# Kernel optimization log

Measured on AMD Instinct MI355X. Metric: run time of the kernel, lower is better.

## Reference

```python
import jax, jax.numpy as jnp
import numpy as np

N_ATOMS = 100000
N_EDGES = 1600000
N_GRAPHS = 64
N_BASIS = 128
N_FILTERS = 128
N_RBF = 32
N_INTER = 6
CUTOFF = 10.0
LOG2 = float(np.log(2.0))


def ssp(x):
    # shifted softplus
    return jax.nn.softplus(x) - LOG2


def setup_inputs() -> dict:
    key = jax.random.key(0)
    ks = jax.random.split(key, 24)
    s = 0.05
    inp = {
        "z": jax.random.randint(ks[0], (N_ATOMS,), 0, 100),
        "z_res": jax.random.randint(ks[1], (N_ATOMS,), 0, 100),
        "pos": jax.random.normal(ks[2], (N_ATOMS, 3), jnp.float32) * 5.0,
        "idx_i": jax.random.randint(ks[3], (N_EDGES,), 0, N_ATOMS),
        "idx_j": jax.random.randint(ks[4], (N_EDGES,), 0, N_ATOMS),
        "edge_attr": jax.random.randint(ks[5], (N_EDGES,), 0, 4),
        "batch": jnp.sort(jax.random.randint(ks[6], (N_ATOMS,), 0, N_GRAPHS)),
        "ele_emb": jax.random.normal(ks[7], (100, N_BASIS), jnp.float32) * s,
        "res_emb": jax.random.normal(ks[8], (100, N_BASIS), jnp.float32) * s,
        "edge_emb": jax.random.normal(ks[9], (4, N_RBF), jnp.float32) * s,
        "in2f_W": jax.random.normal(ks[10], (N_INTER, N_BASIS, N_FILTERS), jnp.float32) * s,
        "filt_W1": jax.random.normal(ks[11], (N_INTER, N_RBF, N_FILTERS), jnp.float32) * s,
        "filt_b1": jnp.zeros((N_INTER, N_FILTERS), jnp.float32),
        "filt_W2": jax.random.normal(ks[12], (N_INTER, N_FILTERS, N_FILTERS), jnp.float32) * s,
        "filt_b2": jnp.zeros((N_INTER, N_FILTERS), jnp.float32),
        "f2out_W1": jax.random.normal(ks[13], (N_INTER, N_FILTERS, N_BASIS), jnp.float32) * s,
        "f2out_b1": jnp.zeros((N_INTER, N_BASIS), jnp.float32),
        "f2out_W2": jax.random.normal(ks[14], (N_INTER, N_BASIS, N_BASIS), jnp.float32) * s,
        "f2out_b2": jnp.zeros((N_INTER, N_BASIS), jnp.float32),
        "head_W1": jax.random.normal(ks[15], (N_BASIS, N_BASIS), jnp.float32) * s,
        "head_b1": jnp.zeros((N_BASIS,), jnp.float32),
        "head_W2": jax.random.normal(ks[16], (N_BASIS, 1), jnp.float32) * s,
    }
    return inp


def _forward(z, z_res, pos, idx_i, idx_j, edge_attr, batch,
             ele_emb, res_emb, edge_emb,
             in2f_W, filt_W1, filt_b1, filt_W2, filt_b2,
             f2out_W1, f2out_b1, f2out_W2, f2out_b2,
             head_W1, head_b1, head_W2):
    # distances per edge
    r_ij = pos[idx_i] - pos[idx_j]                       # [E,3]
    d_ij = jnp.linalg.norm(r_ij, axis=1)                 # [E]

    # Gaussian RBF expansion: offsets linspace(0, cutoff, n_rbf)
    offsets = jnp.linspace(0.0, CUTOFF, N_RBF)
    width = offsets[1] - offsets[0]
    coeff = -0.5 / (width * width)
    f_ij = jnp.exp(coeff * (d_ij[:, None] - offsets[None, :]) ** 2)  # [E,R]
    f_ij = f_ij + edge_emb[edge_attr]

    # cosine cutoff
    rcut_ij = 0.5 * (jnp.cos(d_ij * jnp.pi / CUTOFF) + 1.0) * (d_ij < CUTOFF)

    # atom embeddings
    x = ele_emb[z] + res_emb[z_res]                      # [N,B]

    for i in range(N_INTER):
        xf = x @ in2f_W[i]                               # [N,F]
        Wij = ssp(f_ij @ filt_W1[i] + filt_b1[i]) @ filt_W2[i] + filt_b2[i]
        Wij = Wij * rcut_ij[:, None]                     # [E,F]
        x_ij = xf[idx_j] * Wij                           # gather + multiply
        agg = jax.ops.segment_sum(x_ij, idx_i, num_segments=N_ATOMS)  # scatter_add
        v = ssp(agg @ f2out_W1[i] + f2out_b1[i]) @ f2out_W2[i] + f2out_b2[i]
        x = x + v

    # L2 normalize then head
    h = x / jnp.maximum(jnp.linalg.norm(x, axis=-1, keepdims=True), 1e-12)
    h = jax.nn.silu(h) @ head_W1 + head_b1
    h = jax.nn.silu(h) @ head_W2                         # [N,1]
    new_y = jax.ops.segment_sum(h, batch, num_segments=N_GRAPHS)  # [G,1]
    return new_y.squeeze(-1)


def reference(z, z_res, pos, idx_i, idx_j, edge_attr, batch,
              ele_emb, res_emb, edge_emb,
              in2f_W, filt_W1, filt_b1, filt_W2, filt_b2,
              f2out_W1, f2out_b1, f2out_W2, f2out_b2,
              head_W1, head_b1, head_W2):
    return _forward(z, z_res, pos, idx_i, idx_j, edge_attr, batch,
                    ele_emb, res_emb, edge_emb,
                    in2f_W, filt_W1, filt_b1, filt_W2, filt_b2,
                    f2out_W1, f2out_b1, f2out_W2, f2out_b2,
                    head_W1, head_b1, head_W2)
```

## Files before the change

kernel.cpp:

```cpp
#include <hip/hip_runtime.h>
#include <hip/hip_bf16.h>
#include <math.h>

#define NB 128
#define NR 32
#define EPAD 40
#define HPAD 136
#define SCB 256


static constexpr float CUTOFF_F    = 10.0f;
static constexpr float RBF_STEP    = 10.0f / 31.0f;
static constexpr float RBF_COEFF   = -4.805f;
static constexpr float LOG2_F      = 0.69314718055994531f;
static constexpr float PI_OVER_CUT = 0.314159265358979f;

typedef __attribute__((ext_vector_type(8))) short bf16x8;
typedef __attribute__((ext_vector_type(2))) short bf16x2;
typedef __attribute__((ext_vector_type(4))) float f32x4;

__device__ __forceinline__ short f2bs(float x) {
    __hip_bfloat16 h = __float2bfloat16(x);
    return *reinterpret_cast<short*>(&h);
}
__device__ __forceinline__ float bs2f(unsigned short u) {
    unsigned int v = ((unsigned int)u) << 16;
    return __uint_as_float(v);
}
__device__ __forceinline__ float ssp_f(float v) {
    return fmaxf(v, 0.0f) + __logf(1.0f + __expf(-fabsf(v))) - LOG2_F;
}
__device__ __forceinline__ float silu_f(float v) {
    return v / (1.0f + __expf(-v));
}

__device__ __forceinline__ void atomic_pk_add_bf16(short* addr, float lo, float hi) {
#if __has_builtin(__builtin_amdgcn_global_atomic_fadd_v2bf16)
    typedef bf16x2 __attribute__((address_space(1))) *gptr;
    bf16x2 v;
    v[0] = f2bs(lo);
    v[1] = f2bs(hi);
    __builtin_amdgcn_global_atomic_fadd_v2bf16((gptr)(unsigned long long)addr, v);
#else
    unsigned int* w = (unsigned int*)addr;
    unsigned int old = *w, assumed;
    do {
        assumed = old;
        float fl = bs2f((unsigned short)(assumed & 0xffff)) + lo;
        float fh = bs2f((unsigned short)(assumed >> 16)) + hi;
        unsigned int nv = ((unsigned int)(unsigned short)f2bs(fh) << 16) |
                          (unsigned short)f2bs(fl);
        old = atomicCAS(w, assumed, nv);
    } while (old != assumed);
#endif
}

__device__ __forceinline__ void flush_pk(short* aggrow, const float* accum, int col) {
    bool even = ((col & 1) == 0);
#pragma unroll
    for (int q = 0; q < 4; q++) {
        float a = accum[2 * q], b = accum[2 * q + 1];
        float pa = __shfl_xor(a, 1);
        float pb = __shfl_xor(b, 1);
        int nbase = even ? (2 * q) * 16 + col : (2 * q + 1) * 16 + (col - 1);
        float lo = even ? a : pb;
        float hi = even ? pa : b;
        atomic_pk_add_bf16(aggrow + nbase, lo, hi);
    }
}

__global__ void transpose_cvt(const float* __restrict__ src, short* __restrict__ dst,
                              int R, int C, int total) {
    int t = blockIdx.x * blockDim.x + threadIdx.x;
    if (t >= total) return;
    int rc = R * C;
    int b = t / rc;
    int rem = t - b * rc;
    int c = rem / R;
    int r = rem - c * R;
    dst[t] = f2bs(src[(size_t)b * rc + (size_t)r * C + c]);
}

__global__ void edge_prep4(const float* __restrict__ pos,
                           const int* __restrict__ idx_i,
                           const int* __restrict__ idx_j,
                           float* __restrict__ d_ij,
                           int* __restrict__ hist,
                           int E) {
    int b0 = blockIdx.x * 1024 + threadIdx.x;
    int ia[4], ib[4];
    bool val[4];
#pragma unroll
    for (int k = 0; k < 4; k++) {
        int e = b0 + k * 256;
        val[k] = (e < E);
        ia[k] = val[k] ? idx_i[e] : 0;
        ib[k] = val[k] ? idx_j[e] : 0;
    }
    float ax[4], ay[4], az[4], bx[4], by[4], bz[4];
#pragma unroll
    for (int k = 0; k < 4; k++) {
        const float* pa = pos + ia[k] * 3;
        ax[k] = pa[0]; ay[k] = pa[1]; az[k] = pa[2];
    }
#pragma unroll
    for (int k = 0; k < 4; k++) {
        const float* pb = pos + ib[k] * 3;
        bx[k] = pb[0]; by[k] = pb[1]; bz[k] = pb[2];
    }
#pragma unroll
    for (int k = 0; k < 4; k++) {
        if (!val[k]) continue;
        float dx = ax[k] - bx[k], dy = ay[k] - by[k], dz = az[k] - bz[k];
        float d = sqrtf(dx * dx + dy * dy + dz * dz);
        d_ij[b0 + k * 256] = d;
        if (d < CUTOFF_F) atomicAdd(&hist[ia[k]], 1);
    }
}

__global__ __launch_bounds__(256) void scan_reduce(const int* __restrict__ hist,
                                                   int* __restrict__ partial, int N) {
    __shared__ int red[256];
    int b = blockIdx.x;
    int chunk = (N + SCB - 1) / SCB;
    int lo = b * chunk;
    int hi = min(lo + chunk, N);
    int s = 0;
    for (int i = lo + threadIdx.x; i < hi; i += 256) s += hist[i];
    red[threadIdx.x] = s;
    __syncthreads();
    for (int d = 128; d > 0; d >>= 1) {
        if (threadIdx.x < d) red[threadIdx.x] += red[threadIdx.x + d];
        __syncthreads();
    }
    if (threadIdx.x == 0) partial[b] = red[0];
}

__global__ __launch_bounds__(256) void scan_partials(int* __restrict__ partial) {
    __shared__ int sm[SCB];
    int t = threadIdx.x;
    sm[t] = partial[t];
    __syncthreads();
    for (int d = 1; d < SCB; d <<= 1) {
        int v = (t >= d) ? sm[t - d] : 0;
        __syncthreads();
        sm[t] += v;
        __syncthreads();
    }
    partial[t] = (t == 0) ? 0 : sm[t - 1];
}

__global__ __launch_bounds__(256) void scan_expand(const int* __restrict__ hist,
                                                   const int* __restrict__ partial,
                                                   int* __restrict__ cursor, int N) {
    __shared__ int tsum[256];
    int b = blockIdx.x;
    int chunk = (N + SCB - 1) / SCB;
    int lo = b * chunk;
    int hi = min(lo + chunk, N);
    int sub = (chunk + 255) / 256;
    int tlo = lo + threadIdx.x * sub;
    int thi = min(tlo + sub, hi);
    int s = 0;
    for (int i = tlo; i < thi; i++) s += hist[i];
    int t = threadIdx.x;
    tsum[t] = s;
    __syncthreads();
    for (int d = 1; d < 256; d <<= 1) {
        int v = (t >= d) ? tsum[t - d] : 0;
        __syncthreads();
        tsum[t] += v;
        __syncthreads();
    }
    int run = partial[b] + ((t == 0) ? 0 : tsum[t - 1]);
    for (int i = tlo; i < thi; i++) {
        cursor[i] = run;
        run += hist[i];
    }
}

__global__ void scatter_sorted4(const float* __restrict__ d_ij,
                                const int* __restrict__ idx_i,
                                const int* __restrict__ idx_j,
                                const int* __restrict__ edge_attr,
                                int* __restrict__ cursor,
                                float4* __restrict__ edata,
                                int* __restrict__ sIarr, int E) {
    int b0 = blockIdx.x * 1024 + threadIdx.x;
    float d[4]; int ii[4], jj[4], at[4]; bool act[4];
#pragma unroll
    for (int k = 0; k < 4; k++) {
        int e = b0 + k * 256;
        bool v = (e < E);
        d[k] = v ? d_ij[e] : 1e9f;
        act[k] = (d[k] < CUTOFF_F);
        ii[k] = act[k] ? idx_i[e] : 0;
        jj[k] = act[k] ? idx_j[e] : 0;
        at[k] = act[k] ? edge_attr[e] : 0;
    }
    int p[4];
#pragma unroll
    for (int k = 0; k < 4; k++)
        if (act[k]) p[k] = atomicAdd(&cursor[ii[k]], 1);
#pragma unroll
    for (int k = 0; k < 4; k++) {
        if (!act[k]) continue;
        float4 v;
        v.x = d[k];
        v.y = 0.5f * (__cosf(d[k] * PI_OVER_CUT) + 1.0f);
        v.z = __int_as_float(jj[k]);
        v.w = __int_as_float(at[k]);
        edata[p[k]] = v;
        sIarr[p[k]] = ii[k];
    }
}

__global__ void atom_embed(const int* __restrict__ z,
                           const int* __restrict__ z_res,
                           const float* __restrict__ ele_emb,
                           const float* __restrict__ res_emb,
                           float* __restrict__ x, int N) {
    int t = blockIdx.x * blockDim.x + threadIdx.x;
    if (t >= N * NB) return;
    int n = t >> 7, c = t & 127;
    x[t] = ele_emb[z[n] * NB + c] + res_emb[z_res[n] * NB + c];
}

__global__ __launch_bounds__(256, 4) void node_in2f_mfma(
    const float* __restrict__ x, const short* __restrict__ WT,
    short* __restrict__ xf, int N) {
    __shared__ __align__(16) short XA[64 * HPAD];
    int a0 = blockIdx.x * 64;
    int t = threadIdx.x;
#pragma unroll
    for (int c = 0; c < 4; c++) {
        int chunk = t + c * 256;
        int row = chunk >> 4;
        int col = (chunk & 15) * 8;
        short v[8];
        if (a0 + row < N) {
            const float* src = x + (size_t)(a0 + row) * NB + col;
            float4 f0 = *(const float4*)src;
            float4 f1 = *(const float4*)(src + 4);
            v[0] = f2bs(f0.x); v[1] = f2bs(f0.y); v[2] = f2bs(f0.z); v[3] = f2bs(f0.w);
            v[4] = f2bs(f1.x); v[5] = f2bs(f1.y); v[6] = f2bs(f1.z); v[7] = f2bs(f1.w);
        } else {
#pragma unroll
            for (int j = 0; j < 8; j++) v[j] = 0;
        }
        *(bf16x8*)&XA[row * HPAD + col] = *(bf16x8*)v;
    }
    __syncthreads();

    int wid = t >> 6, lane = t & 63;
    int quad = lane >> 4, col = lane & 15;
    int mrow = wid * 16 + col;

    f32x4 acc[8] = {};
#pragma unroll
    for (int kt = 0; kt < 4; kt++) {
        bf16x8 a = *(bf16x8*)&XA[mrow * HPAD + kt * 32 + quad * 8];
#pragma unroll
        for (int nt = 0; nt < 8; nt++) {
            bf16x8 b = *(const bf16x8*)&WT[(nt * 16 + col) * NB + kt * 32 + quad * 8];
            acc[nt] = __builtin_amdgcn_mfma_f32_16x16x32_bf16(a, b, acc[nt], 0, 0, 0);
        }
    }
#pragma unroll
    for (int nt = 0; nt < 8; nt++) {
        int cst = col * 8 + nt;
#pragma unroll
        for (int r = 0; r < 4; r++) {
            int m = wid * 16 + quad * 4 + r;
            if (a0 + m < N) xf[(size_t)(a0 + m) * NB + cst] = f2bs(acc[nt][r]);
        }
    }
}

__global__ __launch_bounds__(256, 4) void node_fused_mfma(
    short* __restrict__ agg,
    const short* __restrict__ W1T, const float* __restrict__ b1,
    const short* __restrict__ W2T, const float* __restrict__ b2,
    const short* __restrict__ WnT,
    float* __restrict__ x, short* __restrict__ xf, int N) {
    __shared__ __align__(16) short XA[64 * HPAD];
    __shared__ __align__(16) short H[64 * HPAD];
    int a0 = blockIdx.x * 64;
    int t = threadIdx.x;
#pragma unroll
    for (int c = 0; c < 4; c++) {
        int chunk = t + c * 256;
        int row = chunk >> 4;
        int col = (chunk & 15) * 8;
        bf16x8 v = {0, 0, 0, 0, 0, 0, 0, 0};
        if (a0 + row < N) {
            short* src = agg + (size_t)(a0 + row) * NB + col;
            v = *(const bf16x8*)src;
            *(bf16x8*)src = (bf16x8){0, 0, 0, 0, 0, 0, 0, 0};
        }
        *(bf16x8*)&XA[row * HPAD + col] = v;
    }
    __syncthreads();

    int wid = t >> 6, lane = t & 63;
    int quad = lane >> 4, col = lane & 15;
    int mrow = wid * 16 + col;

    {
        f32x4 acc[8] = {};
#pragma unroll
        for (int kt = 0; kt < 4; kt++) {
            bf16x8 a = *(bf16x8*)&XA[mrow * HPAD + kt * 32 + quad * 8];
#pragma unroll
            for (int nt = 0; nt < 8; nt++) {
                bf16x8 b = *(const bf16x8*)&W1T[(nt * 16 + col) * NB + kt * 32 + quad * 8];
                acc[nt] = __builtin_amdgcn_mfma_f32_16x16x32_bf16(a, b, acc[nt], 0, 0, 0);
            }
        }
#pragma unroll
        for (int nt = 0; nt < 8; nt++) {
            int n = nt * 16 + col;
            float bias = b1[n];
#pragma unroll
            for (int r = 0; r < 4; r++) {
                int m = wid * 16 + quad * 4 + r;
                H[m * HPAD + n] = f2bs(ssp_f(acc[nt][r] + bias));
            }
        }
    }
    __syncthreads();

    {
        f32x4 acc[8] = {};
#pragma unroll
        for (int kt = 0; kt < 4; kt++) {
            bf16x8 a = *(bf16x8*)&H[mrow * HPAD + kt * 32 + quad * 8];
#pragma unroll
            for (int nt = 0; nt < 8; nt++) {
                bf16x8 b = *(const bf16x8*)&W2T[(nt * 16 + col) * NB + kt * 32 + quad * 8];
                acc[nt] = __builtin_amdgcn_mfma_f32_16x16x32_bf16(a, b, acc[nt], 0, 0, 0);
            }
        }
#pragma unroll
        for (int nt = 0; nt < 8; nt++) {
            int n = nt * 16 + col;
            float bias = b2[n];
#pragma unroll
            for (int r = 0; r < 4; r++) {
                int m = wid * 16 + quad * 4 + r;
                float xn = 0.0f;
                if (a0 + m < N) {
                    size_t o = (size_t)(a0 + m) * NB + n;
                    xn = x[o] + acc[nt][r] + bias;
                    x[o] = xn;
                }
                XA[m * HPAD + n] = f2bs(xn);
            }
        }
    }
    __syncthreads();

    {
        f32x4 acc[8] = {};
#pragma unroll
        for (int kt = 0; kt < 4; kt++) {
            bf16x8 a = *(bf16x8*)&XA[mrow * HPAD + kt * 32 + quad * 8];
#pragma unroll
            for (int nt = 0; nt < 8; nt++) {
                bf16x8 b = *(const bf16x8*)&WnT[(nt * 16 + col) * NB + kt * 32 + quad * 8];
                acc[nt] = __builtin_amdgcn_mfma_f32_16x16x32_bf16(a, b, acc[nt], 0, 0, 0);
            }
        }
#pragma unroll
        for (int nt = 0; nt < 8; nt++) {
            int cst = col * 8 + nt;
#pragma unroll
            for (int r = 0; r < 4; r++) {
                int m = wid * 16 + quad * 4 + r;
                if (a0 + m < N) xf[(size_t)(a0 + m) * NB + cst] = f2bs(acc[nt][r]);
            }
        }
    }
}

__global__ __launch_bounds__(256, 4) void node_out_head_mfma(
    const short* __restrict__ agg,
    const short* __restrict__ W1T, const float* __restrict__ b1,
    const short* __restrict__ W2T, const float* __restrict__ b2,
    const float* __restrict__ x, const int* __restrict__ batch,
    const short* __restrict__ hW1T, const float* __restrict__ hb1,
    const float* __restrict__ hW2,
    float* __restrict__ out, int N) {
    __shared__ __align__(16) short XA[64 * HPAD];
    __shared__ __align__(16) short H[64 * HPAD];
    __shared__ int sbat[64];
    __shared__ float rowval[64];
    int a0 = blockIdx.x * 64;
    int t = threadIdx.x;

    if (t < 64) sbat[t] = (a0 + t < N) ? batch[a0 + t] : -1;
#pragma unroll
    for (int c = 0; c < 4; c++) {
        int chunk = t + c * 256;
        int row = chunk >> 4;
        int col = (chunk & 15) * 8;
        bf16x8 v = {0, 0, 0, 0, 0, 0, 0, 0};
        if (a0 + row < N) v = *(const bf16x8*)&agg[(size_t)(a0 + row) * NB + col];
        *(bf16x8*)&XA[row * HPAD + col] = v;
    }
    __syncthreads();

    int wid = t >> 6, lane = t & 63;
    int quad = lane >> 4, col = lane & 15;
    int mrow = wid * 16 + col;

    {
        f32x4 acc[8] = {};
#pragma unroll
        for (int kt = 0; kt < 4; kt++) {
            bf16x8 a = *(bf16x8*)&XA[mrow * HPAD + kt * 32 + quad * 8];
#pragma unroll
            for (int nt = 0; nt < 8; nt++) {
                bf16x8 b = *(const bf16x8*)&W1T[(nt * 16 + col) * NB + kt * 32 + quad * 8];
                acc[nt] = __builtin_amdgcn_mfma_f32_16x16x32_bf16(a, b, acc[nt], 0, 0, 0);
            }
        }
#pragma unroll
        for (int nt = 0; nt < 8; nt++) {
            int n = nt * 16 + col;
            float bias = b1[n];
#pragma unroll
            for (int r = 0; r < 4; r++) {
                int m = wid * 16 + quad * 4 + r;
                H[m * HPAD + n] = f2bs(ssp_f(acc[nt][r] + bias));
            }
        }
    }
    __syncthreads();

    float xnv[8][4];
    float ssq[4] = {0.f, 0.f, 0.f, 0.f};
    {
        f32x4 acc[8] = {};
#pragma unroll
        for (int kt = 0; kt < 4; kt++) {
            bf16x8 a = *(bf16x8*)&H[mrow * HPAD + kt * 32 + quad * 8];
#pragma unroll
            for (int nt = 0; nt < 8; nt++) {
                bf16x8 b = *(const bf16x8*)&W2T[(nt * 16 + col) * NB + kt * 32 + quad * 8];
                acc[nt] = __builtin_amdgcn_mfma_f32_16x16x32_bf16(a, b, acc[nt], 0, 0, 0);
            }
        }
#pragma unroll
        for (int nt = 0; nt < 8; nt++) {
            int n = nt * 16 + col;
            float bias = b2[n];
#pragma unroll
            for (int r = 0; r < 4; r++) {
                int m = wid * 16 + quad * 4 + r;
                float xn = 0.0f;
                if (a0 + m < N) xn = x[(size_t)(a0 + m) * NB + n] + acc[nt][r] + bias;
                xnv[nt][r] = xn;
                ssq[r] += xn * xn;
            }
        }
    }
#pragma unroll
    for (int r = 0; r < 4; r++) {
#pragma unroll
        for (int m = 1; m < 16; m <<= 1) ssq[r] += __shfl_xor(ssq[r], m);
    }
    float inv[4];
#pragma unroll
    for (int r = 0; r < 4; r++) inv[r] = 1.0f / fmaxf(sqrtf(ssq[r]), 1e-12f);
    __syncthreads();
#pragma unroll
    for (int nt = 0; nt < 8; nt++) {
        int n = nt * 16 + col;
#pragma unroll
        for (int r = 0; r < 4; r++) {
            int m = wid * 16 + quad * 4 + r;
            XA[m * HPAD + n] = f2bs(silu_f(xnv[nt][r] * inv[r]));
        }
    }
    __syncthreads();

    f32x4 acc[8] = {};
#pragma unroll
    for (int kt = 0; kt < 4; kt++) {
        bf16x8 a = *(bf16x8*)&XA[mrow * HPAD + kt * 32 + quad * 8];
#pragma unroll
        for (int nt = 0; nt < 8; nt++) {
            bf16x8 b = *(const bf16x8*)&hW1T[(nt * 16 + col) * NB + kt * 32 + quad * 8];
            acc[nt] = __builtin_amdgcn_mfma_f32_16x16x32_bf16(a, b, acc[nt], 0, 0, 0);
        }
    }
    float partial[4] = {0.f, 0.f, 0.f, 0.f};
#pragma unroll
    for (int nt = 0; nt < 8; nt++) {
        int n = nt * 16 + col;
        float bias = hb1[n];
        float w2 = hW2[n];
#pragma unroll
        for (int r = 0; r < 4; r++) partial[r] += silu_f(acc[nt][r] + bias) * w2;
    }
#pragma unroll
    for (int r = 0; r < 4; r++) {
#pragma unroll
        for (int d = 1; d < 16; d <<= 1) partial[r] += __shfl_xor(partial[r], d);
    }
    if (col == 0) {
#pragma unroll
        for (int r = 0; r < 4; r++) rowval[wid * 16 + quad * 4 + r] = partial[r];
    }
    __syncthreads();

    if (t < 64) {
        int b = sbat[t];
        bool headf = (b >= 0) && (t == 0 || sbat[t - 1] != b);
        if (headf) {
            float s = 0.0f;
            int rr = t;
            while (rr < 64 && sbat[rr] == b) { s += rowval[rr]; rr++; }
            atomicAdd(&out[b], s);
        }
    }
}

__global__ __launch_bounds__(256, 4) void edge_fused_mfma(
    const float4* __restrict__ edata, const int* __restrict__ sIarr,
    const int* __restrict__ rowend, int natoms,
    const float* __restrict__ edge_emb,
    const short* __restrict__ W1T, const float* __restrict__ b1,
    const short* __restrict__ W2T, const float* __restrict__ b2,
    const short* __restrict__ xf, short* __restrict__ agg) {
    __shared__ __align__(16) short fA[64 * EPAD];
    __shared__ __align__(16) short H[64 * HPAD];

    int t = threadIdx.x;
    int wid = t >> 6, lane = t & 63;
    int quad = lane >> 4, col = lane & 15;
    int base = blockIdx.x * 64;
    int wbase = base + wid * 16;
    int el16 = lane & 15;

    float4 ed = edata[wbase + el16];
    int sIv0 = sIarr[wbase + el16];
    int cnt = rowend[natoms - 1];
    if (base >= cnt) return;

    bool act = (wbase + el16) < cnt;
    float dv  = act ? ed.x : 1e9f;
    float rcv = act ? ed.y : 0.0f;
    int   jjv = act ? __float_as_int(ed.z) : 0;
    int   atv = act ? __float_as_int(ed.w) : 0;
    int   iiv = act ? sIv0 : 0;

    {
        int elA = lane >> 2;
        int r0 = (lane & 3) * 8;
        float d  = __shfl(dv, elA);
        int   at = __shfl(atv, elA);
        const float* em = edge_emb + at * NR + r0;
        short v[8];
#pragma unroll
        for (int j = 0; j < 8; j++) {
            float off = (float)(r0 + j) * RBF_STEP;
            float dd = d - off;
            v[j] = f2bs(__expf(RBF_COEFF * dd * dd) + em[j]);
        }
        *(bf16x8*)&fA[(wid * 16 + elA) * EPAD + r0] = *(bf16x8*)v;
    }

    int e0l = quad * 4;
    bf16x8 xv[4];
    const unsigned short* xg = (const unsigned short*)xf;
#pragma unroll
    for (int r = 0; r < 4; r++) {
        int jj = __shfl(jjv, e0l + r);
        xv[r] = *(const bf16x8*)&xg[(size_t)jj * NB + col * 8];
    }

    asm volatile("s_waitcnt lgkmcnt(0)" ::: "memory");
    __builtin_amdgcn_sched_barrier(0);

    int mrow = wid * 16 + col;

    {
        bf16x8 a1 = *(bf16x8*)&fA[mrow * EPAD + quad * 8];
        f32x4 acc[8];
#pragma unroll
        for (int nt = 0; nt < 8; nt++) {
            bf16x8 b = *(const bf16x8*)&W1T[(nt * 16 + col) * NR + quad * 8];
            acc[nt] = __builtin_amdgcn_mfma_f32_16x16x32_bf16(a1, b, (f32x4){0.f, 0.f, 0.f, 0.f}, 0, 0, 0);
        }
#pragma unroll
        for (int nt = 0; nt < 8; nt++) {
            int n = nt * 16 + col;
            float bias = b1[n];
#pragma unroll
            for (int r = 0; r < 4; r++) {
                int m = wid * 16 + quad * 4 + r;
                H[m * HPAD + n] = f2bs(ssp_f(acc[nt][r] + bias));
            }
        }
    }

    asm volatile("s_waitcnt lgkmcnt(0)" ::: "memory");
    __builtin_amdgcn_sched_barrier(0);

    f32x4 acc2[8] = {};
#pragma unroll
    for (int kt = 0; kt < 4; kt++) {
        bf16x8 a = *(bf16x8*)&H[mrow * HPAD + kt * 32 + quad * 8];
#pragma unroll
        for (int nt = 0; nt < 8; nt++) {
            bf16x8 b = *(const bf16x8*)&W2T[(nt * 16 + col) * NB + kt * 32 + quad * 8];
            acc2[nt] = __builtin_amdgcn_mfma_f32_16x16x32_bf16(a, b, acc2[nt], 0, 0, 0);
        }
    }

    float b2v[8];
#pragma unroll
    for (int nt = 0; nt < 8; nt++) b2v[nt] = b2[nt * 16 + col];

    int cur = __shfl(iiv, e0l);
    float accum[8] = {0.f, 0.f, 0.f, 0.f, 0.f, 0.f, 0.f, 0.f};
#pragma unroll
    for (int r = 0; r < 4; r++) {
        int ii = __shfl(iiv, e0l + r);
        float rc = __shfl(rcv, e0l + r);
        if (ii != cur) {
            flush_pk(agg + (size_t)cur * NB, accum, col);
#pragma unroll
            for (int nt = 0; nt < 8; nt++) accum[nt] = 0.f;
            cur = ii;
        }
#pragma unroll
        for (int nt = 0; nt < 8; nt++) {
            float w = (acc2[nt][r] + b2v[nt]) * rc;
            accum[nt] = fmaf(w, bs2f((unsigned short)xv[r][nt]), accum[nt]);
        }
    }
    flush_pk(agg + (size_t)cur * NB, accum, col);
}

extern "C" void kernel_launch(void* const* d_in, const int* in_sizes, int n_in,
                              void* d_out, int out_size, void* d_ws, size_t ws_size,
                              hipStream_t stream) {
    const int*   z        = (const int*)d_in[0];
    const int*   z_res    = (const int*)d_in[1];
    const float* pos      = (const float*)d_in[2];
    const int*   idx_i    = (const int*)d_in[3];
    const int*   idx_j    = (const int*)d_in[4];
    const int*   edge_attr= (const int*)d_in[5];
    const int*   batch    = (const int*)d_in[6];
    const float* ele_emb  = (const float*)d_in[7];
    const float* res_emb  = (const float*)d_in[8];
    const float* edge_emb = (const float*)d_in[9];
    const float* in2f_W   = (const float*)d_in[10];
    const float* filt_W1  = (const float*)d_in[11];
    const float* filt_b1  = (const float*)d_in[12];
    const float* filt_W2  = (const float*)d_in[13];
    const float* filt_b2  = (const float*)d_in[14];
    const float* f2out_W1 = (const float*)d_in[15];
    const float* f2out_b1 = (const float*)d_in[16];
    const float* f2out_W2 = (const float*)d_in[17];
    const float* f2out_b2 = (const float*)d_in[18];
    const float* head_W1  = (const float*)d_in[19];
    const float* head_b1  = (const float*)d_in[20];
    const float* head_W2  = (const float*)d_in[21];

    const int N = in_sizes[0];
    const int E = in_sizes[3];

    char* p = (char*)d_ws;
    size_t off = 0;
    auto carve = [&](size_t bytes) -> void* {
        void* q = p + off;
        off = (off + bytes + 255) & ~(size_t)255;
        return q;
    };
    float*  d_d      = (float*)carve((size_t)E * 4);
    float4* edata    = (float4*)carve((size_t)E * 16);
    int*    sIarr    = (int*)carve((size_t)E * 4);
    int*    hist     = (int*)carve((size_t)N * 4);
    int*    cursor   = (int*)carve((size_t)N * 4);
    int*    partial  = (int*)carve((size_t)SCB * 4);
    float*  x_buf    = (float*)carve((size_t)N * NB * 4);
    short*  xf_buf   = (short*)carve((size_t)N * NB * 2);
    short*  agg      = (short*)carve((size_t)N * NB * 2);
    short*  in2f_WT  = (short*)carve((size_t)6 * NB * NB * 2);
    short*  fW1T     = (short*)carve((size_t)6 * NR * NB * 2);
    short*  fW2T     = (short*)carve((size_t)6 * NB * NB * 2);
    short*  oW1T     = (short*)carve((size_t)6 * NB * NB * 2);
    short*  oW2T     = (short*)carve((size_t)6 * NB * NB * 2);
    short*  hW1T     = (short*)carve((size_t)NB * NB * 2);
    (void)ws_size;

    {
        int tot = 6 * NB * NB;
        transpose_cvt<<<(tot + 255) / 256, 256, 0, stream>>>(in2f_W, in2f_WT, NB, NB, tot);
        transpose_cvt<<<(tot + 255) / 256, 256, 0, stream>>>(filt_W2, fW2T, NB, NB, tot);
        transpose_cvt<<<(tot + 255) / 256, 256, 0, stream>>>(f2out_W1, oW1T, NB, NB, tot);
        transpose_cvt<<<(tot + 255) / 256, 256, 0, stream>>>(f2out_W2, oW2T, NB, NB, tot);
        int tot1 = 6 * NR * NB;
        transpose_cvt<<<(tot1 + 255) / 256, 256, 0, stream>>>(filt_W1, fW1T, NR, NB, tot1);
        int tot2 = NB * NB;
        transpose_cvt<<<(tot2 + 255) / 256, 256, 0, stream>>>(head_W1, hW1T, NB, NB, tot2);
    }

    hipMemsetAsync(hist, 0, (size_t)N * 4, stream);
    int nblk_e4 = (E + 1023) / 1024;
    edge_prep4<<<nblk_e4, 256, 0, stream>>>(pos, idx_i, idx_j, d_d, hist, E);
    scan_reduce<<<SCB, 256, 0, stream>>>(hist, partial, N);
    scan_partials<<<1, SCB, 0, stream>>>(partial);
    scan_expand<<<SCB, 256, 0, stream>>>(hist, partial, cursor, N);
    scatter_sorted4<<<nblk_e4, 256, 0, stream>>>(d_d, idx_i, idx_j, edge_attr,
                                                 cursor, edata, sIarr, E);

    atom_embed<<<(N * NB + 255) / 256, 256, 0, stream>>>(z, z_res, ele_emb, res_emb, x_buf, N);

    int nblk_atom64 = (N + 63) / 64;
    int nblk_edge = (E + 63) / 64;

    node_in2f_mfma<<<nblk_atom64, 256, 0, stream>>>(x_buf, in2f_WT, xf_buf, N);
    hipMemsetAsync(d_out, 0, (size_t)out_size * sizeof(float), stream);
    hipMemsetAsync(agg, 0, (size_t)N * NB * 2, stream);
    for (int i = 0; i < 6; i++) {
        edge_fused_mfma<<<nblk_edge, 256, 0, stream>>>(
            edata, sIarr, cursor, N, edge_emb,
            fW1T + (size_t)i * NR * NB, filt_b1 + (size_t)i * NB,
            fW2T + (size_t)i * NB * NB, filt_b2 + (size_t)i * NB,
            xf_buf, agg);
        if (i < 5) {
            node_fused_mfma<<<nblk_atom64, 256, 0, stream>>>(
                agg, oW1T + (size_t)i * NB * NB, f2out_b1 + (size_t)i * NB,
                oW2T + (size_t)i * NB * NB, f2out_b2 + (size_t)i * NB,
                in2f_WT + (size_t)(i + 1) * NB * NB,
                x_buf, xf_buf, N);
        } else {
            node_out_head_mfma<<<nblk_atom64, 256, 0, stream>>>(
                agg, oW1T + (size_t)i * NB * NB, f2out_b1 + (size_t)i * NB,
                oW2T + (size_t)i * NB * NB, f2out_b2 + (size_t)i * NB,
                x_buf, batch, hW1T, head_b1, head_W2,
                (float*)d_out, N);
        }
    }
}
```

Measured before the change: 2.208 ms.

## Process 32 edges per wave in edge kernel to reuse weight fragments

Each wave in the fused edge kernel now handles two 16-edge sub-tiles (128 edges per block), loading the W1/W2 B-fragments once and reusing them across both sub-tiles. The goal is to halve the global/cache weight loads per edge and amortize per-block setup. In exchange, register and LDS use roughly double, and launch bounds drop to 3 blocks per CU, which lowers occupancy for a kernel whose gathers are latency-bound.

```diff
diff --git a/kernel.cpp b/kernel.cpp
--- a/kernel.cpp
+++ b/kernel.cpp
@@ -527,29 +527,29 @@
     }
 }
 
-__global__ __launch_bounds__(256, 4) void edge_fused_mfma(
+__global__ __launch_bounds__(256, 3) void edge_fused_mfma(
     const float4* __restrict__ edata, const int* __restrict__ sIarr,
     const int* __restrict__ rowend, int natoms,
     const float* __restrict__ edge_emb,
     const short* __restrict__ W1T, const float* __restrict__ b1,
     const short* __restrict__ W2T, const float* __restrict__ b2,
     const short* __restrict__ xf, short* __restrict__ agg) {
-    __shared__ __align__(16) short fA[64 * EPAD];
-    __shared__ __align__(16) short H[64 * HPAD];
+    __shared__ __align__(16) short fA[128 * EPAD];
+    __shared__ __align__(16) short H[128 * HPAD];
 
     int t = threadIdx.x;
     int wid = t >> 6, lane = t & 63;
     int quad = lane >> 4, col = lane & 15;
-    int base = blockIdx.x * 64;
-    int wbase = base + wid * 16;
-    int el16 = lane & 15;
-
-    float4 ed = edata[wbase + el16];
-    int sIv0 = sIarr[wbase + el16];
+    int base = blockIdx.x * 128;
+    int wbase = base + wid * 32;
+    int el32 = lane & 31;
+
+    float4 ed = edata[wbase + el32];
+    int sIv0 = sIarr[wbase + el32];
     int cnt = rowend[natoms - 1];
     if (base >= cnt) return;
 
-    bool act = (wbase + el16) < cnt;
+    bool act = (wbase + el32) < cnt;
     float dv  = act ? ed.x : 1e9f;
     float rcv = act ? ed.y : 0.0f;
     int   jjv = act ? __float_as_int(ed.z) : 0;
@@ -557,51 +557,58 @@
     int   iiv = act ? sIv0 : 0;
 
     {
-        int elA = lane >> 2;
-        int r0 = (lane & 3) * 8;
+        int elA = lane >> 1;
+        int r0 = (lane & 1) * 16;
         float d  = __shfl(dv, elA);
         int   at = __shfl(atv, elA);
         const float* em = edge_emb + at * NR + r0;
-        short v[8];
-#pragma unroll
-        for (int j = 0; j < 8; j++) {
+        short v[16];
+#pragma unroll
+        for (int j = 0; j < 16; j++) {
             float off = (float)(r0 + j) * RBF_STEP;
             float dd = d - off;
             v[j] = f2bs(__expf(RBF_COEFF * dd * dd) + em[j]);
         }
-        *(bf16x8*)&fA[(wid * 16 + elA) * EPAD + r0] = *(bf16x8*)v;
-    }
-
-    int e0l = quad * 4;
-    bf16x8 xv[4];
+        short* dst = &fA[(wid * 32 + elA) * EPAD + r0];
+        *(bf16x8*)dst = *(bf16x8*)v;
+        *(bf16x8*)(dst + 8) = *(bf16x8*)(v + 8);
+    }
+
+    bf16x8 xv[2][4];
     const unsigned short* xg = (const unsigned short*)xf;
 #pragma unroll
-    for (int r = 0; r < 4; r++) {
-        int jj = __shfl(jjv, e0l + r);
-        xv[r] = *(const bf16x8*)&xg[(size_t)jj * NB + col * 8];
+    for (int s = 0; s < 2; s++) {
+#pragma unroll
+        for (int r = 0; r < 4; r++) {
+            int jj = __shfl(jjv, s * 16 + quad * 4 + r);
+            xv[s][r] = *(const bf16x8*)&xg[(size_t)jj * NB + col * 8];
+        }
     }
 
     asm volatile("s_waitcnt lgkmcnt(0)" ::: "memory");
     __builtin_amdgcn_sched_barrier(0);
 
-    int mrow = wid * 16 + col;
-
     {
-        bf16x8 a1 = *(bf16x8*)&fA[mrow * EPAD + quad * 8];
-        f32x4 acc[8];
-#pragma unroll
-        for (int nt = 0; nt < 8; nt++) {
-            bf16x8 b = *(const bf16x8*)&W1T[(nt * 16 + col) * NR + quad * 8];
-            acc[nt] = __builtin_amdgcn_mfma_f32_16x16x32_bf16(a1, b, (f32x4){0.f, 0.f, 0.f, 0.f}, 0, 0, 0);
-        }
-#pragma unroll
-        for (int nt = 0; nt < 8; nt++) {
-            int n = nt * 16 + col;
-            float bias = b1[n];
-#pragma unroll
-            for (int r = 0; r < 4; r++) {
-                int m = wid * 16 + quad * 4 + r;
-                H[m * HPAD + n] = f2bs(ssp_f(acc[nt][r] + bias));
+        bf16x8 b1f[8];
+#pragma unroll
+        for (int nt = 0; nt < 8; nt++)
+            b1f[nt] = *(const bf16x8*)&W1T[(nt * 16 + col) * NR + quad * 8];
+#pragma unroll
+        for (int s = 0; s < 2; s++) {
+            bf16x8 a1 = *(bf16x8*)&fA[(wid * 32 + s * 16 + col) * EPAD + quad * 8];
+            f32x4 acc[8];
+#pragma unroll
+            for (int nt = 0; nt < 8; nt++)
+                acc[nt] = __builtin_amdgcn_mfma_f32_16x16x32_bf16(a1, b1f[nt], (f32x4){0.f, 0.f, 0.f, 0.f}, 0, 0, 0);
+#pragma unroll
+            for (int nt = 0; nt < 8; nt++) {
+                int n = nt * 16 + col;
+                float bias = b1[n];
+#pragma unroll
+                for (int r = 0; r < 4; r++) {
+                    int m = wid * 32 + s * 16 + quad * 4 + r;
+                    H[m * HPAD + n] = f2bs(ssp_f(acc[nt][r] + bias));
+                }
             }
         }
     }
@@ -609,14 +616,19 @@
     asm volatile("s_waitcnt lgkmcnt(0)" ::: "memory");
     __builtin_amdgcn_sched_barrier(0);
 
-    f32x4 acc2[8] = {};
+    f32x4 acc2[2][8] = {};
 #pragma unroll
     for (int kt = 0; kt < 4; kt++) {
-        bf16x8 a = *(bf16x8*)&H[mrow * HPAD + kt * 32 + quad * 8];
-#pragma unroll
-        for (int nt = 0; nt < 8; nt++) {
-            bf16x8 b = *(const bf16x8*)&W2T[(nt * 16 + col) * NB + kt * 32 + quad * 8];
-            acc2[nt] = __builtin_amdgcn_mfma_f32_16x16x32_bf16(a, b, acc2[nt], 0, 0, 0);
+        bf16x8 b2f[8];
+#pragma unroll
+        for (int nt = 0; nt < 8; nt++)
+            b2f[nt] = *(const bf16x8*)&W2T[(nt * 16 + col) * NB + kt * 32 + quad * 8];
+#pragma unroll
+        for (int s = 0; s < 2; s++) {
+            bf16x8 a = *(bf16x8*)&H[(wid * 32 + s * 16 + col) * HPAD + kt * 32 + quad * 8];
+#pragma unroll
+            for (int nt = 0; nt < 8; nt++)
+                acc2[s][nt] = __builtin_amdgcn_mfma_f32_16x16x32_bf16(a, b2f[nt], acc2[s][nt], 0, 0, 0);
         }
     }
 
@@ -624,25 +636,29 @@
 #pragma unroll
     for (int nt = 0; nt < 8; nt++) b2v[nt] = b2[nt * 16 + col];
 
-    int cur = __shfl(iiv, e0l);
-    float accum[8] = {0.f, 0.f, 0.f, 0.f, 0.f, 0.f, 0.f, 0.f};
-#pragma unroll
-    for (int r = 0; r < 4; r++) {
-        int ii = __shfl(iiv, e0l + r);
-        float rc = __shfl(rcv, e0l + r);
-        if (ii != cur) {
-            flush_pk(agg + (size_t)cur * NB, accum, col);
-#pragma unroll
-            for (int nt = 0; nt < 8; nt++) accum[nt] = 0.f;
-            cur = ii;
-        }
-#pragma unroll
-        for (int nt = 0; nt < 8; nt++) {
-            float w = (acc2[nt][r] + b2v[nt]) * rc;
-            accum[nt] = fmaf(w, bs2f((unsigned short)xv[r][nt]), accum[nt]);
-        }
-    }
-    flush_pk(agg + (size_t)cur * NB, accum, col);
+#pragma unroll
+    for (int s = 0; s < 2; s++) {
+        int e0l = s * 16 + quad * 4;
+        int cur = __shfl(iiv, e0l);
+        float accum[8] = {0.f, 0.f, 0.f, 0.f, 0.f, 0.f, 0.f, 0.f};
+#pragma unroll
+        for (int r = 0; r < 4; r++) {
+            int ii = __shfl(iiv, e0l + r);
+            float rc = __shfl(rcv, e0l + r);
+            if (ii != cur) {
+                flush_pk(agg + (size_t)cur * NB, accum, col);
+#pragma unroll
+                for (int nt = 0; nt < 8; nt++) accum[nt] = 0.f;
+                cur = ii;
+            }
+#pragma unroll
+            for (int nt = 0; nt < 8; nt++) {
+                float w = (acc2[s][nt][r] + b2v[nt]) * rc;
+                accum[nt] = fmaf(w, bs2f((unsigned short)xv[s][r][nt]), accum[nt]);
+            }
+        }
+        flush_pk(agg + (size_t)cur * NB, accum, col);
+    }
 }
 
 extern "C" void kernel_launch(void* const* d_in, const int* in_sizes, int n_in,
@@ -722,7 +738,7 @@
     atom_embed<<<(N * NB + 255) / 256, 256, 0, stream>>>(z, z_res, ele_emb, res_emb, x_buf, N);
 
     int nblk_atom64 = (N + 63) / 64;
-    int nblk_edge = (E + 63) / 64;
+    int nblk_edge = (E + 127) / 128;
 
     node_in2f_mfma<<<nblk_atom64, 256, 0, stream>>>(x_buf, in2f_WT, xf_buf, N);
     hipMemsetAsync(d_out, 0, (size_t)out_size * sizeof(float), stream);
```

Measured after the change: 1.923 ms. 1.15x faster.
